# Optimization experiments

Measured on AMD Instinct MI355X. Metric: run time of the kernel, lower is better.

## Reference

```python
import jax, jax.numpy as jnp
import numpy as np

B, S, IN_DIM, H, D = 2, 2048, 1024, 16, 64

def setup_inputs() -> dict:
    key = jax.random.key(0)
    ks = jax.random.split(key, 8)
    Q = jax.random.normal(ks[0], (B, S, IN_DIM), dtype=jnp.float32)
    K = jax.random.normal(ks[1], (B, S, IN_DIM), dtype=jnp.float32)
    V = jax.random.normal(ks[2], (B, S, IN_DIM), dtype=jnp.float32)
    # True = masked position (matches torch masked_fill_ semantics)
    attn_mask = jax.random.bernoulli(ks[3], 0.1, (B, S, S))
    scale = 1.0 / np.sqrt(IN_DIM)
    Wq = jax.random.normal(ks[4], (IN_DIM, H * D), dtype=jnp.float32) * scale
    Wk = jax.random.normal(ks[5], (IN_DIM, H * D), dtype=jnp.float32) * scale
    Wv = jax.random.normal(ks[6], (IN_DIM, H * D), dtype=jnp.float32) * scale
    Wo = jax.random.normal(ks[7], (H * D, IN_DIM), dtype=jnp.float32) * scale
    return {"Q": Q, "K": K, "V": V, "attn_mask": attn_mask,
            "Wq": Wq, "Wk": Wk, "Wv": Wv, "Wo": Wo}

def reference(Q, K, V, attn_mask, Wq, Wk, Wv, Wo):
    b, s, _ = Q.shape
    # Projections -> [B, H, S, D]
    q = (Q @ Wq).reshape(b, s, H, D).transpose(0, 2, 1, 3)
    k = (K @ Wk).reshape(b, s, H, D).transpose(0, 2, 1, 3)
    v = (V @ Wv).reshape(b, s, H, D).transpose(0, 2, 1, 3)
    scores = jnp.einsum('bhqd,bhkd->bhqk', q, k) / np.sqrt(D)
    scores = jnp.where(attn_mask[:, None, :, :], jnp.float32(-1e9), scores)
    attn = jax.nn.softmax(scores, axis=-1)
    ctx = jnp.einsum('bhqk,bhkd->bhqd', attn, v)  # [B, H, S, D]
    ctx = ctx.transpose(0, 2, 1, 3).reshape(b, s, H * D)
    return ctx @ Wo + Q
```

## Files before the change

### kernel.cpp

```cpp
#include <hip/hip_runtime.h>
#include <hip/hip_bf16.h>


#define BB   2
#define SS   2048
#define IND  1024
#define HH   16
#define DD   64
#define MM_ELEMS 524288

typedef __attribute__((ext_vector_type(8))) short  s8b;
typedef __attribute__((ext_vector_type(4))) short  s4b;
typedef __attribute__((ext_vector_type(4))) float  f32x4;

static __device__ __forceinline__ short f2b(float x) {
    return __builtin_bit_cast(short, __float2bfloat16(x));
}

#define GLD16(g, l)                                                             \
    __builtin_amdgcn_global_load_lds(                                           \
        (const __attribute__((address_space(1))) unsigned int*)(g),             \
        (__attribute__((address_space(3))) unsigned int*)(l), 16, 0, 0)

__global__ __launch_bounds__(256) void wconv(const float* __restrict__ w0,
                                             const float* __restrict__ w1,
                                             const float* __restrict__ w2,
                                             const float* __restrict__ w3,
                                             short* __restrict__ out) {
    const int z = blockIdx.z;
    const float* src = (z == 0) ? w0 : (z == 1) ? w1 : (z == 2) ? w2 : w3;
    const float wscale = (z == 0) ? 0.125f : 1.0f;
    short* dst = out + (size_t)z * IND * IND;
    __shared__ __attribute__((aligned(16))) short ls[64][72];
    const int t  = threadIdx.x;
    const int k0 = blockIdx.y * 64;
    const int n0 = blockIdx.x * 64;
#pragma unroll
    for (int p = 0; p < 4; ++p) {
        int ch = t + p * 256;
        int r  = ch >> 4;
        int c4 = ch & 15;
        float4 v = *reinterpret_cast<const float4*>(&src[(size_t)(k0 + r) * IND + n0 + c4 * 4]);
        ls[r][c4 * 4 + 0] = f2b(v.x * wscale);
        ls[r][c4 * 4 + 1] = f2b(v.y * wscale);
        ls[r][c4 * 4 + 2] = f2b(v.z * wscale);
        ls[r][c4 * 4 + 3] = f2b(v.w * wscale);
    }
    __syncthreads();
#pragma unroll
    for (int p = 0; p < 2; ++p) {
        int ch = t + p * 256;
        int nr = ch >> 3;
        int kg = ch & 7;
        s8b o;
#pragma unroll
        for (int j = 0; j < 8; ++j) o[j] = ls[kg * 8 + j][nr];
        *reinterpret_cast<s8b*>(&dst[(size_t)(n0 + nr) * IND + k0 + kg * 8]) = o;
    }
}

__global__ __launch_bounds__(256) void maskpack(const unsigned char* __restrict__ mask,
                                                unsigned long long* __restrict__ bits) {
    __shared__ int s_flag;
    const int t = threadIdx.x;
    if (t == 0) s_flag = 0;
    __syncthreads();
    {
        int bad = 0;
#pragma unroll
        for (int i = 0; i < 16; ++i) {
            int idx = t * 16 + i;
            if ((idx & 3) && mask[idx]) bad = 1;
        }
        if (bad) s_flag = 1;
    }
    __syncthreads();
    const bool isI32 = (s_flag == 0);

    const int lane = t & 63;
    const size_t nwords = (size_t)BB * SS * SS / 64;
    size_t w = (size_t)blockIdx.x * 4 + (t >> 6);
    const size_t stride = (size_t)gridDim.x * 4;
    if (isI32) {
        const unsigned* m4 = (const unsigned*)mask;
        for (; w < nwords; w += stride) {
            unsigned long long bal = __ballot(m4[w * 64 + lane] != 0);
            if (lane == 0) bits[w] = bal;
        }
    } else {
        for (; w < nwords; w += stride) {
            unsigned long long bal = __ballot(mask[w * 64 + lane] != 0);
            if (lane == 0) bits[w] = bal;
        }
    }
}

__global__ __launch_bounds__(256) void cvt3(const float* __restrict__ q,
                                            const float* __restrict__ k,
                                            const float* __restrict__ v,
                                            short* __restrict__ o) {
    const size_t nchunk = (size_t)3 * MM_ELEMS;
    size_t i = (size_t)blockIdx.x * 256 + threadIdx.x;
    const size_t stride = (size_t)gridDim.x * 256;
    for (; i < nchunk; i += stride) {
        size_t base = i * 8;
        int z = (int)(base >> 22);
        size_t off = base & 4194303u;
        const float* src = (z == 0) ? q : (z == 1) ? k : v;
        float4 a = *reinterpret_cast<const float4*>(&src[off]);
        float4 b = *reinterpret_cast<const float4*>(&src[off + 4]);
        s8b w;
        w[0] = f2b(a.x); w[1] = f2b(a.y); w[2] = f2b(a.z); w[3] = f2b(a.w);
        w[4] = f2b(b.x); w[5] = f2b(b.y); w[6] = f2b(b.z); w[7] = f2b(b.w);
        *reinterpret_cast<s8b*>(&o[base]) = w;
    }
}

__global__ __launch_bounds__(256) void gemm_qkv(const short* __restrict__ abf,
                                                const short* __restrict__ wt,
                                                short* __restrict__ qb,
                                                short* __restrict__ kb,
                                                short* __restrict__ vt) {
    __shared__ __attribute__((aligned(16))) short lsA[128 * 40];
    __shared__ __attribute__((aligned(16))) short lsB[128 * 40];
    const int z = blockIdx.z;
    const short* A  = abf + (size_t)z * 4194304;
    const short* Bt = wt + (size_t)z * IND * IND;

    const int t    = threadIdx.x;
    const int lane = t & 63;
    const int wv   = t >> 6;
    const int wr   = wv >> 1, wc = wv & 1;
    const int m0   = blockIdx.y * 128, n0 = blockIdx.x * 128;
    const int lr   = lane & 15;
    const int lg   = lane >> 4;

    f32x4 acc[4][4] = {};

    for (int k0 = 0; k0 < IND; k0 += 32) {
        __syncthreads();
#pragma unroll
        for (int p = 0; p < 2; ++p) {
            int ch = t + p * 256;
            int r = ch >> 2, c8 = ch & 3;
            s8b v = *reinterpret_cast<const s8b*>(&A[(size_t)(m0 + r) * IND + k0 + c8 * 8]);
            *reinterpret_cast<s8b*>(&lsA[r * 40 + c8 * 8]) = v;
        }
#pragma unroll
        for (int p = 0; p < 2; ++p) {
            int ch = t + p * 256;
            int r = ch >> 2, c8 = ch & 3;
            s8b v = *reinterpret_cast<const s8b*>(&Bt[(size_t)(n0 + r) * IND + k0 + c8 * 8]);
            *reinterpret_cast<s8b*>(&lsB[r * 40 + c8 * 8]) = v;
        }
        __syncthreads();

        s8b af[4], bfr[4];
#pragma unroll
        for (int mi = 0; mi < 4; ++mi)
            af[mi] = *reinterpret_cast<const s8b*>(&lsA[(wr * 64 + mi * 16 + lr) * 40 + lg * 8]);
#pragma unroll
        for (int nj = 0; nj < 4; ++nj)
            bfr[nj] = *reinterpret_cast<const s8b*>(&lsB[(wc * 64 + nj * 16 + lr) * 40 + lg * 8]);
#pragma unroll
        for (int mi = 0; mi < 4; ++mi)
#pragma unroll
            for (int nj = 0; nj < 4; ++nj)
                acc[mi][nj] = __builtin_amdgcn_mfma_f32_16x16x32_bf16(af[mi], bfr[nj], acc[mi][nj], 0, 0, 0);
    }

#pragma unroll
    for (int mi = 0; mi < 4; ++mi) {
#pragma unroll
        for (int nj = 0; nj < 4; ++nj) {
            const int mbase = m0 + wr * 64 + mi * 16 + lg * 4;
            const int n     = n0 + wc * 64 + nj * 16 + lr;
            if (z < 2) {
                short* o = z ? kb : qb;
                const int h = n >> 6, d = n & 63;
#pragma unroll
                for (int i = 0; i < 4; ++i) {
                    int m = mbase + i;
                    int b = m >> 11, s = m & 2047;
                    o[((size_t)(b * HH + h) * SS + s) * DD + d] = f2b(acc[mi][nj][i]);
                }
            } else {
                const int b = mbase >> 11, sbase = mbase & 2047;
                const int h = n >> 6, d = n & 63;
                s4b w;
#pragma unroll
                for (int i = 0; i < 4; ++i) w[i] = f2b(acc[mi][nj][i]);
                *reinterpret_cast<s4b*>(&vt[((size_t)(b * HH + h) * DD + d) * SS + sbase]) = w;
            }
        }
    }
}

__global__ __launch_bounds__(256) void attn(const short* __restrict__ qb,
                                            const short* __restrict__ kb,
                                            const short* __restrict__ vt,
                                            const unsigned* __restrict__ mbw,
                                            short* __restrict__ ctx) {
    __shared__ __attribute__((aligned(16))) short lsK[2][64 * 64];
    __shared__ __attribute__((aligned(16))) short lsV[2][64 * 64];
    __shared__ __attribute__((aligned(16))) short lsP[4][16 * 72];

    const int t    = threadIdx.x;
    const int lane = t & 63;
    const int wv   = t >> 6;
    const int bh   = blockIdx.y;
    const int b    = bh >> 4, h = bh & 15;
    const int q0   = blockIdx.x * 64 + wv * 16;
    const int lr   = lane & 15;
    const int lg   = lane >> 4;

    const unsigned sel0 = 1u << lr;
    const unsigned sel1 = sel0 << 16;
    const uint2* mrp = (const uint2*)(mbw + (size_t)(b * SS + q0 + lg * 4) * (SS / 32));

    const int rk = lane >> 3;
    const int ck = (lane & 7) ^ rk;
    const short* kbase = kb + (size_t)bh * SS * DD;
    const short* vbase = vt + (size_t)bh * DD * SS;

    s8b aq[2];
#pragma unroll
    for (int ks = 0; ks < 2; ++ks)
        aq[ks] = *reinterpret_cast<const s8b*>(&qb[((size_t)bh * SS + q0 + lr) * DD + ks * 32 + lg * 8]);

    s8b ones;
#pragma unroll
    for (int j = 0; j < 8; ++j) ones[j] = (short)0x3F80;

    f32x4 o[4] = {};
    float lrow[4] = {0.f, 0.f, 0.f, 0.f};

#pragma unroll
    for (int c = 0; c < 2; ++c) {
        int chunk = wv + c * 4;
        int row = chunk * 8 + rk;
        GLD16(&kbase[(size_t)row * DD + ck * 8], &lsK[0][chunk * 512]);
        GLD16(&vbase[(size_t)row * SS + ck * 8], &lsV[0][chunk * 512]);
    }

    int cur = 0;
    for (int kk0 = 0; kk0 < SS; kk0 += 64) {
        uint2 mw[4];
#pragma unroll
        for (int i = 0; i < 4; ++i) mw[i] = mrp[i * 32 + (kk0 >> 6)];

        __syncthreads();

        if (kk0 + 64 < SS) {
#pragma unroll
            for (int c = 0; c < 2; ++c) {
                int chunk = wv + c * 4;
                int row = chunk * 8 + rk;
                GLD16(&kbase[(size_t)(kk0 + 64 + row) * DD + ck * 8], &lsK[cur ^ 1][chunk * 512]);
                GLD16(&vbase[(size_t)row * SS + kk0 + 64 + ck * 8], &lsV[cur ^ 1][chunk * 512]);
            }
        }

        const short* Kc = lsK[cur];
        const short* Vc = lsV[cur];

        f32x4 sc[4];
#pragma unroll
        for (int nj = 0; nj < 4; ++nj) {
            const int R  = nj * 16 + lr;
            const int sw = R & 7;
            s8b bk0 = *reinterpret_cast<const s8b*>(&Kc[R * 64 + ((lg ^ sw) << 3)]);
            s8b bk1 = *reinterpret_cast<const s8b*>(&Kc[R * 64 + (((lg ^ 4) ^ sw) << 3)]);
            f32x4 zz = {};
            zz     = __builtin_amdgcn_mfma_f32_16x16x32_bf16(aq[0], bk0, zz, 0, 0, 0);
            sc[nj] = __builtin_amdgcn_mfma_f32_16x16x32_bf16(aq[1], bk1, zz, 0, 0, 0);
        }

#pragma unroll
        for (int nj = 0; nj < 4; ++nj) {
            const unsigned slm = (nj & 1) ? sel1 : sel0;
#pragma unroll
            for (int i = 0; i < 4; ++i) {
                unsigned w = (nj < 2) ? mw[i].x : mw[i].y;
                float e = __expf(sc[nj][i]);
                float p = (w & slm) ? 0.f : e;
                lsP[wv][(lg * 4 + i) * 72 + nj * 16 + lr] = f2b(p);
            }
        }

        s8b pa[2];
#pragma unroll
        for (int ks = 0; ks < 2; ++ks)
            pa[ks] = *reinterpret_cast<const s8b*>(&lsP[wv][lr * 72 + ks * 32 + lg * 8]);

        f32x4 rs = {};
        rs = __builtin_amdgcn_mfma_f32_16x16x32_bf16(pa[0], ones, rs, 0, 0, 0);
        rs = __builtin_amdgcn_mfma_f32_16x16x32_bf16(pa[1], ones, rs, 0, 0, 0);

#pragma unroll
        for (int nj = 0; nj < 4; ++nj) {
            const int R  = nj * 16 + lr;
            const int sw = R & 7;
            s8b bv0 = *reinterpret_cast<const s8b*>(&Vc[R * 64 + ((lg ^ sw) << 3)]);
            s8b bv1 = *reinterpret_cast<const s8b*>(&Vc[R * 64 + (((lg ^ 4) ^ sw) << 3)]);
            o[nj] = __builtin_amdgcn_mfma_f32_16x16x32_bf16(pa[0], bv0, o[nj], 0, 0, 0);
            o[nj] = __builtin_amdgcn_mfma_f32_16x16x32_bf16(pa[1], bv1, o[nj], 0, 0, 0);
        }
#pragma unroll
        for (int i = 0; i < 4; ++i) lrow[i] += rs[i];

        cur ^= 1;
    }

    float inv[4];
#pragma unroll
    for (int i = 0; i < 4; ++i) inv[i] = 1.0f / lrow[i];
#pragma unroll
    for (int nj = 0; nj < 4; ++nj)
#pragma unroll
        for (int i = 0; i < 4; ++i) {
            int q = q0 + lg * 4 + i;
            ctx[((size_t)(b * SS + q)) * (HH * DD) + h * DD + nj * 16 + lr] = f2b(o[nj][i] * inv[i]);
        }
}

__global__ __launch_bounds__(256) void gemm_out(const short* __restrict__ Actx,
                                                const short* __restrict__ Bt,
                                                const float* __restrict__ resid,
                                                float* __restrict__ outp) {
    __shared__ __attribute__((aligned(16))) short lsA[64 * 40];
    __shared__ __attribute__((aligned(16))) short lsB[128 * 40];
    const int t    = threadIdx.x;
    const int lane = t & 63;
    const int wv   = t >> 6;
    const int wr   = wv >> 1, wc = wv & 1;
    const int m0   = blockIdx.y * 64, n0 = blockIdx.x * 128;
    const int lr   = lane & 15;
    const int lg   = lane >> 4;

    f32x4 acc[2][4] = {};

    for (int k0 = 0; k0 < IND; k0 += 32) {
        __syncthreads();
        {
            int r = t >> 2, c8 = t & 3;
            s8b v = *reinterpret_cast<const s8b*>(&Actx[(size_t)(m0 + r) * IND + k0 + c8 * 8]);
            *reinterpret_cast<s8b*>(&lsA[r * 40 + c8 * 8]) = v;
        }
#pragma unroll
        for (int p = 0; p < 2; ++p) {
            int ch = t + p * 256;
            int r = ch >> 2, c8 = ch & 3;
            s8b v = *reinterpret_cast<const s8b*>(&Bt[(size_t)(n0 + r) * IND + k0 + c8 * 8]);
            *reinterpret_cast<s8b*>(&lsB[r * 40 + c8 * 8]) = v;
        }
        __syncthreads();

        s8b af[2], bfr[4];
#pragma unroll
        for (int mi = 0; mi < 2; ++mi)
            af[mi] = *reinterpret_cast<const s8b*>(&lsA[(wr * 32 + mi * 16 + lr) * 40 + lg * 8]);
#pragma unroll
        for (int nj = 0; nj < 4; ++nj)
            bfr[nj] = *reinterpret_cast<const s8b*>(&lsB[(wc * 64 + nj * 16 + lr) * 40 + lg * 8]);
#pragma unroll
        for (int mi = 0; mi < 2; ++mi)
#pragma unroll
            for (int nj = 0; nj < 4; ++nj)
                acc[mi][nj] = __builtin_amdgcn_mfma_f32_16x16x32_bf16(af[mi], bfr[nj], acc[mi][nj], 0, 0, 0);
    }

#pragma unroll
    for (int mi = 0; mi < 2; ++mi)
#pragma unroll
        for (int nj = 0; nj < 4; ++nj) {
            const int mbase = m0 + wr * 32 + mi * 16 + lg * 4;
            const int n     = n0 + wc * 64 + nj * 16 + lr;
#pragma unroll
            for (int i = 0; i < 4; ++i) {
                int m = mbase + i;
                outp[(size_t)m * IND + n] = acc[mi][nj][i] + resid[(size_t)m * IND + n];
            }
        }
}

extern "C" void kernel_launch(void* const* d_in, const int* in_sizes, int n_in,
                              void* d_out, int out_size, void* d_ws, size_t ws_size,
                              hipStream_t stream) {
    const float* Qin = (const float*)d_in[0];
    const float* Kin = (const float*)d_in[1];
    const float* Vin = (const float*)d_in[2];
    const unsigned char* mask = (const unsigned char*)d_in[3];
    const float* Wq = (const float*)d_in[4];
    const float* Wk = (const float*)d_in[5];
    const float* Wv = (const float*)d_in[6];
    const float* Wo = (const float*)d_in[7];

    char* ws = (char*)d_ws;
    const size_t WSZ = (size_t)IND * IND;
    short* wt  = (short*)ws;
    short* qb  = (short*)(ws + 8ull  * 1024 * 1024);
    short* kb  = (short*)(ws + 16ull * 1024 * 1024);
    short* vt  = (short*)(ws + 24ull * 1024 * 1024);
    unsigned long long* mbits = (unsigned long long*)(ws + 32ull * 1024 * 1024);
    short* abf = (short*)(ws + 36ull * 1024 * 1024);
    short* ctx = (short*)(ws + 36ull * 1024 * 1024);

    wconv   <<<dim3(16, 16, 4), 256, 0, stream>>>(Wq, Wk, Wv, Wo, wt);
    maskpack<<<512, 256, 0, stream>>>(mask, mbits);
    cvt3    <<<2048, 256, 0, stream>>>(Qin, Kin, Vin, abf);
    gemm_qkv<<<dim3(8, 32, 3), 256, 0, stream>>>(abf, wt, qb, kb, vt);
    attn    <<<dim3(SS / 64, BB * HH), 256, 0, stream>>>(qb, kb, vt, (const unsigned*)mbits, ctx);
    gemm_out<<<dim3(8, 64), 256, 0, stream>>>(ctx, wt + 3 * WSZ, Qin, (float*)d_out);
}
```

Measured before the change: 328.9 us.

## Use direct global-to-LDS loads in GEMMs and single-buffer attention K/V

Both projection GEMMs now stage A and B tiles with global_load_lds DMA instead of register round-trips, with the LDS row stride cut from 40 to 32 shorts because the DMA writes contiguous 64-lane chunks. The goal is to save VGPRs and the load/store instruction pair per tile. The attention kernel drops K/V double buffering for a single buffer, loading the next tile after an extra barrier at the end of each iteration. This halves its LDS use to raise occupancy, but it loses the overlap between prefetch and compute. The unpadded stride of 32 may also bring LDS bank conflicts on the fragment reads.

```diff
diff --git a/kernel.cpp b/kernel.cpp
--- a/kernel.cpp
+++ b/kernel.cpp
@@ -121,8 +121,8 @@
                                                 short* __restrict__ qb,
                                                 short* __restrict__ kb,
                                                 short* __restrict__ vt) {
-    __shared__ __attribute__((aligned(16))) short lsA[128 * 40];
-    __shared__ __attribute__((aligned(16))) short lsB[128 * 40];
+    __shared__ __attribute__((aligned(16))) short lsA[128 * 32];
+    __shared__ __attribute__((aligned(16))) short lsB[128 * 32];
     const int z = blockIdx.z;
     const short* A  = abf + (size_t)z * 4194304;
     const short* Bt = wt + (size_t)z * IND * IND;
@@ -134,34 +134,26 @@
     const int m0   = blockIdx.y * 128, n0 = blockIdx.x * 128;
     const int lr   = lane & 15;
     const int lg   = lane >> 4;
+    const int rs   = lane >> 2;
+    const int cs   = lane & 3;
 
     f32x4 acc[4][4] = {};
 
     for (int k0 = 0; k0 < IND; k0 += 32) {
         __syncthreads();
-#pragma unroll
-        for (int p = 0; p < 2; ++p) {
-            int ch = t + p * 256;
-            int r = ch >> 2, c8 = ch & 3;
-            s8b v = *reinterpret_cast<const s8b*>(&A[(size_t)(m0 + r) * IND + k0 + c8 * 8]);
-            *reinterpret_cast<s8b*>(&lsA[r * 40 + c8 * 8]) = v;
-        }
-#pragma unroll
-        for (int p = 0; p < 2; ++p) {
-            int ch = t + p * 256;
-            int r = ch >> 2, c8 = ch & 3;
-            s8b v = *reinterpret_cast<const s8b*>(&Bt[(size_t)(n0 + r) * IND + k0 + c8 * 8]);
-            *reinterpret_cast<s8b*>(&lsB[r * 40 + c8 * 8]) = v;
-        }
+        GLD16(&A [(size_t)(m0 + wv * 16      + rs) * IND + k0 + cs * 8], &lsA[ wv      * 512]);
+        GLD16(&A [(size_t)(m0 + (wv+4) * 16  + rs) * IND + k0 + cs * 8], &lsA[(wv + 4) * 512]);
+        GLD16(&Bt[(size_t)(n0 + wv * 16      + rs) * IND + k0 + cs * 8], &lsB[ wv      * 512]);
+        GLD16(&Bt[(size_t)(n0 + (wv+4) * 16  + rs) * IND + k0 + cs * 8], &lsB[(wv + 4) * 512]);
         __syncthreads();
 
         s8b af[4], bfr[4];
 #pragma unroll
         for (int mi = 0; mi < 4; ++mi)
-            af[mi] = *reinterpret_cast<const s8b*>(&lsA[(wr * 64 + mi * 16 + lr) * 40 + lg * 8]);
+            af[mi] = *reinterpret_cast<const s8b*>(&lsA[(wr * 64 + mi * 16 + lr) * 32 + lg * 8]);
 #pragma unroll
         for (int nj = 0; nj < 4; ++nj)
-            bfr[nj] = *reinterpret_cast<const s8b*>(&lsB[(wc * 64 + nj * 16 + lr) * 40 + lg * 8]);
+            bfr[nj] = *reinterpret_cast<const s8b*>(&lsB[(wc * 64 + nj * 16 + lr) * 32 + lg * 8]);
 #pragma unroll
         for (int mi = 0; mi < 4; ++mi)
 #pragma unroll
@@ -201,8 +193,8 @@
                                             const short* __restrict__ vt,
                                             const unsigned* __restrict__ mbw,
                                             short* __restrict__ ctx) {
-    __shared__ __attribute__((aligned(16))) short lsK[2][64 * 64];
-    __shared__ __attribute__((aligned(16))) short lsV[2][64 * 64];
+    __shared__ __attribute__((aligned(16))) short lsK[64 * 64];
+    __shared__ __attribute__((aligned(16))) short lsV[64 * 64];
     __shared__ __attribute__((aligned(16))) short lsP[4][16 * 72];
 
     const int t    = threadIdx.x;
@@ -239,11 +231,10 @@
     for (int c = 0; c < 2; ++c) {
         int chunk = wv + c * 4;
         int row = chunk * 8 + rk;
-        GLD16(&kbase[(size_t)row * DD + ck * 8], &lsK[0][chunk * 512]);
-        GLD16(&vbase[(size_t)row * SS + ck * 8], &lsV[0][chunk * 512]);
-    }
-
-    int cur = 0;
+        GLD16(&kbase[(size_t)row * DD + ck * 8], &lsK[chunk * 512]);
+        GLD16(&vbase[(size_t)row * SS + ck * 8], &lsV[chunk * 512]);
+    }
+
     for (int kk0 = 0; kk0 < SS; kk0 += 64) {
         uint2 mw[4];
 #pragma unroll
@@ -251,26 +242,13 @@
 
         __syncthreads();
 
-        if (kk0 + 64 < SS) {
-#pragma unroll
-            for (int c = 0; c < 2; ++c) {
-                int chunk = wv + c * 4;
-                int row = chunk * 8 + rk;
-                GLD16(&kbase[(size_t)(kk0 + 64 + row) * DD + ck * 8], &lsK[cur ^ 1][chunk * 512]);
-                GLD16(&vbase[(size_t)row * SS + kk0 + 64 + ck * 8], &lsV[cur ^ 1][chunk * 512]);
-            }
-        }
-
-        const short* Kc = lsK[cur];
-        const short* Vc = lsV[cur];
-
         f32x4 sc[4];
 #pragma unroll
         for (int nj = 0; nj < 4; ++nj) {
             const int R  = nj * 16 + lr;
             const int sw = R & 7;
-            s8b bk0 = *reinterpret_cast<const s8b*>(&Kc[R * 64 + ((lg ^ sw) << 3)]);
-            s8b bk1 = *reinterpret_cast<const s8b*>(&Kc[R * 64 + (((lg ^ 4) ^ sw) << 3)]);
+            s8b bk0 = *reinterpret_cast<const s8b*>(&lsK[R * 64 + ((lg ^ sw) << 3)]);
+            s8b bk1 = *reinterpret_cast<const s8b*>(&lsK[R * 64 + (((lg ^ 4) ^ sw) << 3)]);
             f32x4 zz = {};
             zz     = __builtin_amdgcn_mfma_f32_16x16x32_bf16(aq[0], bk0, zz, 0, 0, 0);
             sc[nj] = __builtin_amdgcn_mfma_f32_16x16x32_bf16(aq[1], bk1, zz, 0, 0, 0);
@@ -301,15 +279,25 @@
         for (int nj = 0; nj < 4; ++nj) {
             const int R  = nj * 16 + lr;
             const int sw = R & 7;
-            s8b bv0 = *reinterpret_cast<const s8b*>(&Vc[R * 64 + ((lg ^ sw) << 3)]);
-            s8b bv1 = *reinterpret_cast<const s8b*>(&Vc[R * 64 + (((lg ^ 4) ^ sw) << 3)]);
+            s8b bv0 = *reinterpret_cast<const s8b*>(&lsV[R * 64 + ((lg ^ sw) << 3)]);
+            s8b bv1 = *reinterpret_cast<const s8b*>(&lsV[R * 64 + (((lg ^ 4) ^ sw) << 3)]);
             o[nj] = __builtin_amdgcn_mfma_f32_16x16x32_bf16(pa[0], bv0, o[nj], 0, 0, 0);
             o[nj] = __builtin_amdgcn_mfma_f32_16x16x32_bf16(pa[1], bv1, o[nj], 0, 0, 0);
         }
 #pragma unroll
         for (int i = 0; i < 4; ++i) lrow[i] += rs[i];
 
-        cur ^= 1;
+        __syncthreads();
+
+        if (kk0 + 64 < SS) {
+#pragma unroll
+            for (int c = 0; c < 2; ++c) {
+                int chunk = wv + c * 4;
+                int row = chunk * 8 + rk;
+                GLD16(&kbase[(size_t)(kk0 + 64 + row) * DD + ck * 8], &lsK[chunk * 512]);
+                GLD16(&vbase[(size_t)row * SS + kk0 + 64 + ck * 8], &lsV[chunk * 512]);
+            }
+        }
     }
 
     float inv[4];
@@ -328,8 +316,8 @@
                                                 const short* __restrict__ Bt,
                                                 const float* __restrict__ resid,
                                                 float* __restrict__ outp) {
-    __shared__ __attribute__((aligned(16))) short lsA[64 * 40];
-    __shared__ __attribute__((aligned(16))) short lsB[128 * 40];
+    __shared__ __attribute__((aligned(16))) short lsA[64 * 32];
+    __shared__ __attribute__((aligned(16))) short lsB[128 * 32];
     const int t    = threadIdx.x;
     const int lane = t & 63;
     const int wv   = t >> 6;
@@ -337,32 +325,25 @@
     const int m0   = blockIdx.y * 64, n0 = blockIdx.x * 128;
     const int lr   = lane & 15;
     const int lg   = lane >> 4;
+    const int rs   = lane >> 2;
+    const int cs   = lane & 3;
 
     f32x4 acc[2][4] = {};
 
     for (int k0 = 0; k0 < IND; k0 += 32) {
         __syncthreads();
-        {
-            int r = t >> 2, c8 = t & 3;
-            s8b v = *reinterpret_cast<const s8b*>(&Actx[(size_t)(m0 + r) * IND + k0 + c8 * 8]);
-            *reinterpret_cast<s8b*>(&lsA[r * 40 + c8 * 8]) = v;
-        }
-#pragma unroll
-        for (int p = 0; p < 2; ++p) {
-            int ch = t + p * 256;
-            int r = ch >> 2, c8 = ch & 3;
-            s8b v = *reinterpret_cast<const s8b*>(&Bt[(size_t)(n0 + r) * IND + k0 + c8 * 8]);
-            *reinterpret_cast<s8b*>(&lsB[r * 40 + c8 * 8]) = v;
-        }
+        GLD16(&Actx[(size_t)(m0 + wv * 16     + rs) * IND + k0 + cs * 8], &lsA[ wv      * 512]);
+        GLD16(&Bt  [(size_t)(n0 + wv * 16     + rs) * IND + k0 + cs * 8], &lsB[ wv      * 512]);
+        GLD16(&Bt  [(size_t)(n0 + (wv+4) * 16 + rs) * IND + k0 + cs * 8], &lsB[(wv + 4) * 512]);
         __syncthreads();
 
         s8b af[2], bfr[4];
 #pragma unroll
         for (int mi = 0; mi < 2; ++mi)
-            af[mi] = *reinterpret_cast<const s8b*>(&lsA[(wr * 32 + mi * 16 + lr) * 40 + lg * 8]);
+            af[mi] = *reinterpret_cast<const s8b*>(&lsA[(wr * 32 + mi * 16 + lr) * 32 + lg * 8]);
 #pragma unroll
         for (int nj = 0; nj < 4; ++nj)
-            bfr[nj] = *reinterpret_cast<const s8b*>(&lsB[(wc * 64 + nj * 16 + lr) * 40 + lg * 8]);
+            bfr[nj] = *reinterpret_cast<const s8b*>(&lsB[(wc * 64 + nj * 16 + lr) * 32 + lg * 8]);
 #pragma unroll
         for (int mi = 0; mi < 2; ++mi)
 #pragma unroll
```

Result: faster. 293.3 us (-10.8%).
